# Optimization experiments

Measured on AMD Instinct MI355X. Metric: run time of the kernel, lower is better.

## Reference

```python
import jax, jax.numpy as jnp
import numpy as np

N1, D1 = 16, 64
IN_SPECS = [(512, 8), (512, 8)]  # (num_in_caps, dim_in_caps) per input layer
TOTAL_IN = sum(n for n, _ in IN_SPECS)
B = 16
EPS = 1e-5


def _kaiming_normal(key, shape):
    # kaiming_normal_(mode='fan_in', nonlinearity='relu'): std = sqrt(2/fan_in)
    # For a 4D tensor [N1, num_in, dim_in, D1], torch fan_in = dim_in * D1
    fan_in = shape[2] * shape[3]
    std = np.sqrt(2.0 / fan_in)
    return jax.random.normal(key, shape, dtype=jnp.float32) * std


def setup_inputs() -> dict:
    key = jax.random.key(0)
    ks = jax.random.split(key, 2 + len(IN_SPECS))
    x0 = jax.random.normal(ks[0], (B, IN_SPECS[0][0], IN_SPECS[0][1]), dtype=jnp.float32)
    x1 = jax.random.normal(ks[1], (B, IN_SPECS[1][0], IN_SPECS[1][1]), dtype=jnp.float32)
    W0 = _kaiming_normal(ks[2], (N1, IN_SPECS[0][0], IN_SPECS[0][1], D1))
    W1 = _kaiming_normal(ks[3], (N1, IN_SPECS[1][0], IN_SPECS[1][1], D1))
    b = jnp.zeros((N1, TOTAL_IN, TOTAL_IN), dtype=jnp.float32)
    return {"x0": x0, "x1": x1, "W0": W0, "W1": W1, "b": b}


def _squash(x):
    sq = jnp.sum(x * x, axis=-1, keepdims=True)  # squared norm
    return (sq / (1.0 + sq)) * x / (jnp.sqrt(sq) + EPS)


def reference(x0, x1, W0, W1, b):
    # Per-input capsule projections: [B,i,j] x [k,i,j,l] -> [B,k,i,l]
    U0 = jnp.einsum('bij,kijl->bkil', x0, W0)
    U1 = jnp.einsum('bij,kijl->bkil', x1, W1)
    U = jnp.concatenate([U0, U1], axis=2)  # [B, N1, TOTAL_IN, D1]
    scale = jnp.sqrt(jnp.asarray(D1, dtype=jnp.float32))
    # Attention-like agreement matrix: [B, N1, TOTAL_IN, TOTAL_IN]
    A = jnp.einsum('bkil,bkzl->bkiz', U, U) / scale
    C = jax.nn.softmax(A, axis=-1) + b  # post-softmax learned additive bias
    # S[b,k,l] = sum_i sum_z U[b,k,i,l] * C[b,k,i,z]  (contracts both i and z)
    S = jnp.einsum('bkil,bki->bkl', U, jnp.sum(C, axis=-1))  # [B, N1, D1]
    return _squash(S)
```

## Files before the change

### kernel.cpp

```cpp
#include <hip/hip_runtime.h>


__global__ __launch_bounds__(256, 4) void proj_kernel(
        const float* __restrict__ x0, const float* __restrict__ x1,
        const float* __restrict__ W0, const float* __restrict__ W1,
        const float* __restrict__ bias, float* __restrict__ partial) {
    __shared__ float xs[16 * 132];
    __shared__ float ssum[16];
    __shared__ float rbuf[4 * 8 * 64];
    const int tid = threadIdx.x;
    const int k     = blockIdx.x >> 6;
    const int chunk = blockIdx.x & 63;
    const int g  = tid >> 4;
    const int q  = tid & 15;
    const int w  = tid >> 6;
    const int gw = g & 3;

    const int layer = chunk >> 5;
    const int i0    = (chunk & 31) * 16;
    const int ig0   = chunk * 16;
    const float* __restrict__ x = layer ? x1 : x0;
    const float* __restrict__ W = layer ? W1 : W0;

    const float4* xp = (const float4*)(x + (size_t)(g * 512 + i0 + q) * 8);
    float4 a0 = xp[0], a1 = xp[1];

    const float4* bp = (const float4*)(bias + (size_t)(k * 1024 + ig0 + g) * 1024);
    float4 va[8], vb[8];
#pragma unroll
    for (int it = 0; it < 8; ++it) va[it] = bp[q + 16 * it];
#pragma unroll
    for (int it = 0; it < 8; ++it) vb[it] = bp[q + 16 * (8 + it)];

    const float4* Wf4 = (const float4*)W;
    const size_t wbase = (size_t)(k * 512 + i0 + g) * 128 + q;
    float4 wv[8];
#pragma unroll
    for (int j = 0; j < 8; ++j) wv[j] = Wf4[wbase + j * 16];
    __builtin_amdgcn_sched_barrier(0);

    {
        float s0 = 0.f, s1 = 0.f, s2 = 0.f, s3 = 0.f;
#pragma unroll
        for (int it = 0; it < 8; it += 4) {
            s0 += va[it].x + va[it].y + va[it].z + va[it].w;
            s1 += va[it + 1].x + va[it + 1].y + va[it + 1].z + va[it + 1].w;
            s2 += va[it + 2].x + va[it + 2].y + va[it + 2].z + va[it + 2].w;
            s3 += va[it + 3].x + va[it + 3].y + va[it + 3].z + va[it + 3].w;
        }
#pragma unroll
        for (int it = 0; it < 8; it += 4) {
            s0 += vb[it].x + vb[it].y + vb[it].z + vb[it].w;
            s1 += vb[it + 1].x + vb[it + 1].y + vb[it + 1].z + vb[it + 1].w;
            s2 += vb[it + 2].x + vb[it + 2].y + vb[it + 2].z + vb[it + 2].w;
            s3 += vb[it + 3].x + vb[it + 3].y + vb[it + 3].z + vb[it + 3].w;
        }
        float s = (s0 + s1) + (s2 + s3);
#pragma unroll
        for (int m = 8; m >= 1; m >>= 1) s += __shfl_xor(s, m);
        if (q == 0) ssum[g] = 1.0f + s;
    }
    asm volatile("s_waitcnt lgkmcnt(0)" ::: "memory");
    __builtin_amdgcn_s_barrier();
    __builtin_amdgcn_sched_barrier(0);

    {
        const float s = ssum[q];
        *(float4*)&xs[q * 132 + g * 8] =
            make_float4(a0.x * s, a0.y * s, a0.z * s, a0.w * s);
        *(float4*)&xs[q * 132 + g * 8 + 4] =
            make_float4(a1.x * s, a1.y * s, a1.z * s, a1.w * s);
    }
    asm volatile("s_waitcnt lgkmcnt(0)" ::: "memory");
    __builtin_amdgcn_s_barrier();
    __builtin_amdgcn_sched_barrier(0);

#pragma unroll
    for (int half = 0; half < 2; ++half) {
        float4 acc[8];
#pragma unroll
        for (int bi = 0; bi < 8; ++bi) acc[bi] = make_float4(0.f, 0.f, 0.f, 0.f);
#pragma unroll
        for (int bi = 0; bi < 8; ++bi) {
            const int b = half * 8 + bi;
            float xr[8];
            *(float4*)&xr[0] = *(const float4*)&xs[g * 132 + b * 8];
            *(float4*)&xr[4] = *(const float4*)&xs[g * 132 + b * 8 + 4];
#pragma unroll
            for (int j = 0; j < 8; ++j) {
                acc[bi].x += xr[j] * wv[j].x;
                acc[bi].y += xr[j] * wv[j].y;
                acc[bi].z += xr[j] * wv[j].z;
                acc[bi].w += xr[j] * wv[j].w;
            }
        }
#pragma unroll
        for (int bi = 0; bi < 8; ++bi) {
            acc[bi].x += __shfl_xor(acc[bi].x, 32); acc[bi].x += __shfl_xor(acc[bi].x, 16);
            acc[bi].y += __shfl_xor(acc[bi].y, 32); acc[bi].y += __shfl_xor(acc[bi].y, 16);
            acc[bi].z += __shfl_xor(acc[bi].z, 32); acc[bi].z += __shfl_xor(acc[bi].z, 16);
            acc[bi].w += __shfl_xor(acc[bi].w, 32); acc[bi].w += __shfl_xor(acc[bi].w, 16);
        }
        if (gw == 0) {
#pragma unroll
            for (int bi = 0; bi < 8; ++bi)
                *(float4*)&rbuf[(w * 8 + bi) * 64 + q * 4] = acc[bi];
        }
        __syncthreads();
        {
            const int bi = tid >> 5;
            const int l  = tid & 31;
            float v0 = 0.f, v1 = 0.f;
#pragma unroll
            for (int ww = 0; ww < 4; ++ww) {
                v0 += rbuf[(ww * 8 + bi) * 64 + l];
                v1 += rbuf[(ww * 8 + bi) * 64 + l + 32];
            }
            const int b = half * 8 + bi;
            partial[(size_t)blockIdx.x * 1024 + b * 64 + l]      = v0;
            partial[(size_t)blockIdx.x * 1024 + b * 64 + l + 32] = v1;
        }
        __syncthreads();
    }
}

__global__ __launch_bounds__(256) void reduce_squash_kernel(
        const float* __restrict__ partial, float* __restrict__ out) {
    __shared__ float red[4][64];
    const int row = blockIdx.x;
    const int b = row >> 4, k = row & 15;
    const int w = threadIdx.x >> 6, lane = threadIdx.x & 63;
    float s = 0.f;
#pragma unroll
    for (int cc = 0; cc < 16; ++cc) {
        const int c = w + cc * 4;
        s += partial[((size_t)(k * 64 + c)) * 1024 + b * 64 + lane];
    }
    red[w][lane] = s;
    __syncthreads();
    if (w == 0) {
        float v = red[0][lane] + red[1][lane] + red[2][lane] + red[3][lane];
        float sq = v * v;
#pragma unroll
        for (int m = 32; m >= 1; m >>= 1) sq += __shfl_xor(sq, m);
        out[(size_t)row * 64 + lane] = (sq / (1.0f + sq)) * v / (sqrtf(sq) + 1e-5f);
    }
}

extern "C" void kernel_launch(void* const* d_in, const int* in_sizes, int n_in,
                              void* d_out, int out_size, void* d_ws, size_t ws_size,
                              hipStream_t stream) {
    const float* x0  = (const float*)d_in[0];
    const float* x1  = (const float*)d_in[1];
    const float* W0  = (const float*)d_in[2];
    const float* W1  = (const float*)d_in[3];
    const float* bia = (const float*)d_in[4];
    float* out = (float*)d_out;

    float* partial = (float*)d_ws;

    proj_kernel<<<dim3(1024), dim3(256), 0, stream>>>(x0, x1, W0, W1, bia, partial);
    reduce_squash_kernel<<<dim3(256), dim3(256), 0, stream>>>(partial, out);
}
```

Before: 27.55 us.

## Process two capsule chunks per block and prefetch the second chunk's loads

Each block now handles two consecutive 16-capsule chunks, halving the grid to 512 blocks. The bias rows and W tile for the second chunk are loaded into registers while the first chunk is being computed, so their memory latency is hidden behind useful work. The price is much higher register pressure: the occupancy hint in launch_bounds is dropped, and fewer waves per CU may cut latency hiding. Plain __syncthreads calls are replaced by explicit lgkmcnt waits followed by a barrier.

```diff
diff --git a/kernel.cpp b/kernel.cpp
--- a/kernel.cpp
+++ b/kernel.cpp
@@ -1,42 +1,52 @@
 #include <hip/hip_runtime.h>
 
 
-__global__ __launch_bounds__(256, 4) void proj_kernel(
+#define LGKM_BARRIER()                                        \
+    do {                                                      \
+        asm volatile("s_waitcnt lgkmcnt(0)" ::: "memory");    \
+        __builtin_amdgcn_s_barrier();                         \
+        __builtin_amdgcn_sched_barrier(0);                    \
+    } while (0)
+
+__global__ __launch_bounds__(256) void proj_kernel(
         const float* __restrict__ x0, const float* __restrict__ x1,
         const float* __restrict__ W0, const float* __restrict__ W1,
         const float* __restrict__ bias, float* __restrict__ partial) {
-    __shared__ float xs[16 * 132];
-    __shared__ float ssum[16];
+    __shared__ float xs[2][16 * 132];
+    __shared__ float ssum[32];
     __shared__ float rbuf[4 * 8 * 64];
     const int tid = threadIdx.x;
-    const int k     = blockIdx.x >> 6;
-    const int chunk = blockIdx.x & 63;
+    const int k  = blockIdx.x >> 5;
+    const int cp = blockIdx.x & 31;
     const int g  = tid >> 4;
     const int q  = tid & 15;
     const int w  = tid >> 6;
     const int gw = g & 3;
 
-    const int layer = chunk >> 5;
-    const int i0    = (chunk & 31) * 16;
-    const int ig0   = chunk * 16;
+    const int c0    = cp * 2;
+    const int layer = c0 >> 5;
+    const int i0    = (c0 & 31) * 16;
+    const int ig0   = c0 * 16;
     const float* __restrict__ x = layer ? x1 : x0;
     const float* __restrict__ W = layer ? W1 : W0;
 
-    const float4* xp = (const float4*)(x + (size_t)(g * 512 + i0 + q) * 8);
-    float4 a0 = xp[0], a1 = xp[1];
-
-    const float4* bp = (const float4*)(bias + (size_t)(k * 1024 + ig0 + g) * 1024);
+    const float4* xpa = (const float4*)(x + (size_t)(g * 512 + i0 + q) * 8);
+    float4 a0 = xpa[0], a1 = xpa[1];
+    const float4* xpb = (const float4*)(x + (size_t)(g * 512 + i0 + 16 + q) * 8);
+    float4 a2 = xpb[0], a3 = xpb[1];
+
+    const float4* bp0 = (const float4*)(bias + (size_t)(k * 1024 + ig0 + g) * 1024);
     float4 va[8], vb[8];
 #pragma unroll
-    for (int it = 0; it < 8; ++it) va[it] = bp[q + 16 * it];
-#pragma unroll
-    for (int it = 0; it < 8; ++it) vb[it] = bp[q + 16 * (8 + it)];
+    for (int it = 0; it < 8; ++it) va[it] = bp0[q + 16 * it];
+#pragma unroll
+    for (int it = 0; it < 8; ++it) vb[it] = bp0[q + 16 * (8 + it)];
 
     const float4* Wf4 = (const float4*)W;
-    const size_t wbase = (size_t)(k * 512 + i0 + g) * 128 + q;
-    float4 wv[8];
-#pragma unroll
-    for (int j = 0; j < 8; ++j) wv[j] = Wf4[wbase + j * 16];
+    const size_t wb0 = (size_t)(k * 512 + i0 + g) * 128 + q;
+    float4 wv0[8];
+#pragma unroll
+    for (int j = 0; j < 8; ++j) wv0[j] = Wf4[wb0 + j * 16];
     __builtin_amdgcn_sched_barrier(0);
 
     {
@@ -60,20 +70,28 @@
         for (int m = 8; m >= 1; m >>= 1) s += __shfl_xor(s, m);
         if (q == 0) ssum[g] = 1.0f + s;
     }
-    asm volatile("s_waitcnt lgkmcnt(0)" ::: "memory");
-    __builtin_amdgcn_s_barrier();
+    LGKM_BARRIER();
+
+    {
+        const float s = ssum[q];
+        *(float4*)&xs[0][q * 132 + g * 8] =
+            make_float4(a0.x * s, a0.y * s, a0.z * s, a0.w * s);
+        *(float4*)&xs[0][q * 132 + g * 8 + 4] =
+            make_float4(a1.x * s, a1.y * s, a1.z * s, a1.w * s);
+    }
+
+    const float4* bp1 = bp0 + 4096;
+    float4 u0[8], u1[8];
+#pragma unroll
+    for (int it = 0; it < 8; ++it) u0[it] = bp1[q + 16 * it];
+#pragma unroll
+    for (int it = 0; it < 8; ++it) u1[it] = bp1[q + 16 * (8 + it)];
+    const size_t wb1 = wb0 + 16 * 128;
+    float4 wv1[8];
+#pragma unroll
+    for (int j = 0; j < 8; ++j) wv1[j] = Wf4[wb1 + j * 16];
     __builtin_amdgcn_sched_barrier(0);
-
-    {
-        const float s = ssum[q];
-        *(float4*)&xs[q * 132 + g * 8] =
-            make_float4(a0.x * s, a0.y * s, a0.z * s, a0.w * s);
-        *(float4*)&xs[q * 132 + g * 8 + 4] =
-            make_float4(a1.x * s, a1.y * s, a1.z * s, a1.w * s);
-    }
-    asm volatile("s_waitcnt lgkmcnt(0)" ::: "memory");
-    __builtin_amdgcn_s_barrier();
-    __builtin_amdgcn_sched_barrier(0);
+    LGKM_BARRIER();
 
 #pragma unroll
     for (int half = 0; half < 2; ++half) {
@@ -84,14 +102,14 @@
         for (int bi = 0; bi < 8; ++bi) {
             const int b = half * 8 + bi;
             float xr[8];
-            *(float4*)&xr[0] = *(const float4*)&xs[g * 132 + b * 8];
-            *(float4*)&xr[4] = *(const float4*)&xs[g * 132 + b * 8 + 4];
+            *(float4*)&xr[0] = *(const float4*)&xs[0][g * 132 + b * 8];
+            *(float4*)&xr[4] = *(const float4*)&xs[0][g * 132 + b * 8 + 4];
 #pragma unroll
             for (int j = 0; j < 8; ++j) {
-                acc[bi].x += xr[j] * wv[j].x;
-                acc[bi].y += xr[j] * wv[j].y;
-                acc[bi].z += xr[j] * wv[j].z;
-                acc[bi].w += xr[j] * wv[j].w;
+                acc[bi].x += xr[j] * wv0[j].x;
+                acc[bi].y += xr[j] * wv0[j].y;
+                acc[bi].z += xr[j] * wv0[j].z;
+                acc[bi].w += xr[j] * wv0[j].w;
             }
         }
 #pragma unroll
@@ -106,7 +124,7 @@
             for (int bi = 0; bi < 8; ++bi)
                 *(float4*)&rbuf[(w * 8 + bi) * 64 + q * 4] = acc[bi];
         }
-        __syncthreads();
+        LGKM_BARRIER();
         {
             const int bi = tid >> 5;
             const int l  = tid & 31;
@@ -117,10 +135,90 @@
                 v1 += rbuf[(ww * 8 + bi) * 64 + l + 32];
             }
             const int b = half * 8 + bi;
-            partial[(size_t)blockIdx.x * 1024 + b * 64 + l]      = v0;
-            partial[(size_t)blockIdx.x * 1024 + b * 64 + l + 32] = v1;
-        }
-        __syncthreads();
+            partial[((size_t)(k * 64 + c0)) * 1024 + b * 64 + l]      = v0;
+            partial[((size_t)(k * 64 + c0)) * 1024 + b * 64 + l + 32] = v1;
+        }
+        LGKM_BARRIER();
+    }
+
+    {
+        float s0 = 0.f, s1 = 0.f, s2 = 0.f, s3 = 0.f;
+#pragma unroll
+        for (int it = 0; it < 8; it += 4) {
+            s0 += u0[it].x + u0[it].y + u0[it].z + u0[it].w;
+            s1 += u0[it + 1].x + u0[it + 1].y + u0[it + 1].z + u0[it + 1].w;
+            s2 += u0[it + 2].x + u0[it + 2].y + u0[it + 2].z + u0[it + 2].w;
+            s3 += u0[it + 3].x + u0[it + 3].y + u0[it + 3].z + u0[it + 3].w;
+        }
+#pragma unroll
+        for (int it = 0; it < 8; it += 4) {
+            s0 += u1[it].x + u1[it].y + u1[it].z + u1[it].w;
+            s1 += u1[it + 1].x + u1[it + 1].y + u1[it + 1].z + u1[it + 1].w;
+            s2 += u1[it + 2].x + u1[it + 2].y + u1[it + 2].z + u1[it + 2].w;
+            s3 += u1[it + 3].x + u1[it + 3].y + u1[it + 3].z + u1[it + 3].w;
+        }
+        float s = (s0 + s1) + (s2 + s3);
+#pragma unroll
+        for (int m = 8; m >= 1; m >>= 1) s += __shfl_xor(s, m);
+        if (q == 0) ssum[16 + g] = 1.0f + s;
+    }
+    LGKM_BARRIER();
+
+    {
+        const float s = ssum[16 + q];
+        *(float4*)&xs[1][q * 132 + g * 8] =
+            make_float4(a2.x * s, a2.y * s, a2.z * s, a2.w * s);
+        *(float4*)&xs[1][q * 132 + g * 8 + 4] =
+            make_float4(a3.x * s, a3.y * s, a3.z * s, a3.w * s);
+    }
+    LGKM_BARRIER();
+
+#pragma unroll
+    for (int half = 0; half < 2; ++half) {
+        float4 acc[8];
+#pragma unroll
+        for (int bi = 0; bi < 8; ++bi) acc[bi] = make_float4(0.f, 0.f, 0.f, 0.f);
+#pragma unroll
+        for (int bi = 0; bi < 8; ++bi) {
+            const int b = half * 8 + bi;
+            float xr[8];
+            *(float4*)&xr[0] = *(const float4*)&xs[1][g * 132 + b * 8];
+            *(float4*)&xr[4] = *(const float4*)&xs[1][g * 132 + b * 8 + 4];
+#pragma unroll
+            for (int j = 0; j < 8; ++j) {
+                acc[bi].x += xr[j] * wv1[j].x;
+                acc[bi].y += xr[j] * wv1[j].y;
+                acc[bi].z += xr[j] * wv1[j].z;
+                acc[bi].w += xr[j] * wv1[j].w;
+            }
+        }
+#pragma unroll
+        for (int bi = 0; bi < 8; ++bi) {
+            acc[bi].x += __shfl_xor(acc[bi].x, 32); acc[bi].x += __shfl_xor(acc[bi].x, 16);
+            acc[bi].y += __shfl_xor(acc[bi].y, 32); acc[bi].y += __shfl_xor(acc[bi].y, 16);
+            acc[bi].z += __shfl_xor(acc[bi].z, 32); acc[bi].z += __shfl_xor(acc[bi].z, 16);
+            acc[bi].w += __shfl_xor(acc[bi].w, 32); acc[bi].w += __shfl_xor(acc[bi].w, 16);
+        }
+        if (gw == 0) {
+#pragma unroll
+            for (int bi = 0; bi < 8; ++bi)
+                *(float4*)&rbuf[(w * 8 + bi) * 64 + q * 4] = acc[bi];
+        }
+        LGKM_BARRIER();
+        {
+            const int bi = tid >> 5;
+            const int l  = tid & 31;
+            float v0 = 0.f, v1 = 0.f;
+#pragma unroll
+            for (int ww = 0; ww < 4; ++ww) {
+                v0 += rbuf[(ww * 8 + bi) * 64 + l];
+                v1 += rbuf[(ww * 8 + bi) * 64 + l + 32];
+            }
+            const int b = half * 8 + bi;
+            partial[((size_t)(k * 64 + c0 + 1)) * 1024 + b * 64 + l]      = v0;
+            partial[((size_t)(k * 64 + c0 + 1)) * 1024 + b * 64 + l + 32] = v1;
+        }
+        LGKM_BARRIER();
     }
 }
 
@@ -159,6 +257,6 @@
 
     float* partial = (float*)d_ws;
 
-    proj_kernel<<<dim3(1024), dim3(256), 0, stream>>>(x0, x1, W0, W1, bia, partial);
+    proj_kernel<<<dim3(512), dim3(256), 0, stream>>>(x0, x1, W0, W1, bia, partial);
     reduce_squash_kernel<<<dim3(256), dim3(256), 0, stream>>>(partial, out);
 }
```

Result: slower. 29.45 us (+6.9%).
